# Kernel optimization log

Measured on AMD Instinct MI355X. Metric: run time of the kernel, lower is better.

The kernel has to match this reference:

```python
import jax, jax.numpy as jnp
import numpy as np

B, S, E = 4, 2048, 1024

def setup_inputs() -> dict:
    key = jax.random.key(0)
    ks = jax.random.split(key, 9)
    lim = 1.0 / np.sqrt(E)
    inp = {
        "query": jax.random.normal(ks[0], (B, S, E), dtype=jnp.float32),
        "key": jax.random.normal(ks[1], (B, S, E), dtype=jnp.float32),
        "value": jax.random.normal(ks[2], (B, S, E), dtype=jnp.float32),
        "Wq": jax.random.uniform(ks[3], (E, E), jnp.float32, -lim, lim),
        "bq": jax.random.uniform(ks[4], (E,), jnp.float32, -lim, lim),
        "Wk": jax.random.uniform(ks[5], (E, E), jnp.float32, -lim, lim),
        "bk": jax.random.uniform(ks[6], (E,), jnp.float32, -lim, lim),
        "Wv": jax.random.uniform(ks[7], (E, E), jnp.float32, -lim, lim),
        "bv": jax.random.uniform(ks[8], (E,), jnp.float32, -lim, lim),
    }
    return inp

def reference(query, key, value, Wq, bq, Wk, bk, Wv, bv):
    # Linear layers (torch stores weight as [out,in]; here W is [in,out] used as x @ W)
    q = query @ Wq + bq            # [B,S,E]
    k = key @ Wk + bk              # [B,S,E]
    v = value @ Wv + bv            # [B,S,E]
    inv_scale = jnp.asarray(E, q.dtype) ** 0.5
    scores = jnp.einsum("bse,bte->bst", q, k) / inv_scale  # [B,S,S]
    attn = jax.nn.softmax(scores, axis=-1)
    # dropout_p = 0.0 -> identity
    out = jnp.einsum("bst,bte->bse", attn, v)  # [B,S,E]
    return out
```

## Files before the change

### kernel.cpp

```cpp
#include <hip/hip_runtime.h>
#include <hip/hip_bf16.h>


typedef __bf16 bf16_t;
typedef bf16_t bf16x8 __attribute__((ext_vector_type(8)));
typedef bf16_t bf16x4 __attribute__((ext_vector_type(4)));
typedef float  f32x4  __attribute__((ext_vector_type(4)));

typedef const __attribute__((address_space(1))) unsigned gl_uint;
typedef __attribute__((address_space(3))) unsigned lds_uint;

#define BM 128
#define BN 128
#define BK 64

__device__ __forceinline__ void gload_lds16(const void* g, void* l) {
  __builtin_amdgcn_global_load_lds((gl_uint*)g, (lds_uint*)l, 16, 0, 0);
}

__device__ __forceinline__ void mfma_tile(const bf16_t* As, const bf16_t* Bs,
                                          f32x4 acc[4][4]) {
  const int lane = threadIdx.x & 63;
  const int quad = lane >> 4;
  const int l15  = lane & 15;
  const int wid  = threadIdx.x >> 6;
  const int wm   = (wid >> 1) * 64;
  const int wn   = (wid & 1) * 64;
  const int csw  = l15 & 7;
#pragma unroll
  for (int ks = 0; ks < 2; ++ks) {
    const int sg = ks * 4 + quad;
    const int c  = (sg ^ csw) * 8;
    bf16x8 fa[4], fb[4];
#pragma unroll
    for (int i = 0; i < 4; ++i)
      fa[i] = *(const bf16x8*)&As[(wm + i * 16 + l15) * BK + c];
#pragma unroll
    for (int i = 0; i < 4; ++i)
      fb[i] = *(const bf16x8*)&Bs[(wn + i * 16 + l15) * BK + c];
#pragma unroll
    for (int mi = 0; mi < 4; ++mi)
#pragma unroll
      for (int ni = 0; ni < 4; ++ni)
        acc[mi][ni] = __builtin_amdgcn_mfma_f32_16x16x32_bf16(
            fa[mi], fb[ni], acc[mi][ni], 0, 0, 0);
  }
}

__device__ __forceinline__ void gemm_core_bf16(
    const bf16_t* __restrict__ Ab, const bf16_t* __restrict__ Bb,
    const int K, bf16_t* As, bf16_t* Bs, f32x4 acc[4][4])
{
  const int tid = threadIdx.x;
  for (int kt = 0; kt < K; kt += BK) {
#pragma unroll
    for (int j = 0; j < 4; ++j) {
      const int lin = j * 256 + tid;
      const int row = lin >> 3;
      const int seg = (lin & 7) ^ (row & 7);
      gload_lds16(Ab + (size_t)row * K + kt + seg * 8, &As[lin * 8]);
    }
#pragma unroll
    for (int j = 0; j < 4; ++j) {
      const int lin = j * 256 + tid;
      const int row = lin >> 3;
      const int seg = (lin & 7) ^ (row & 7);
      gload_lds16(Bb + (size_t)row * K + kt + seg * 8, &Bs[lin * 8]);
    }
    __syncthreads();
    mfma_tile(As, Bs, acc);
    __syncthreads();
  }
}

__global__ __launch_bounds__(256, 2)
void qkv_proj(const float* __restrict__ q, const float* __restrict__ k,
              const float* __restrict__ v, const bf16_t* __restrict__ Wqt,
              const bf16_t* __restrict__ Wkt, const bf16_t* __restrict__ Wvt,
              const float* __restrict__ bq, const float* __restrict__ bk,
              const float* __restrict__ bv, bf16_t* __restrict__ qp,
              bf16_t* __restrict__ kp, bf16_t* __restrict__ vT)
{
  __shared__ __align__(16) bf16_t As[BM * BK];
  __shared__ __align__(16) bf16_t Bs[BN * BK];

  const int L = blockIdx.x;
  const int g = L >> 3;
  const int gst = (L & 7) * 3 + (g >> 6);
  const int z  = gst >> 3;
  const int sy = gst & 7;
  const int w  = g & 63;
  const int bx = w & 7;
  const int by = sy * 8 + (w >> 3);

  const float*  A    = (z == 0) ? q : (z == 1) ? k : v;
  const bf16_t* W    = (z == 0) ? Wqt : (z == 1) ? Wkt : Wvt;
  const float*  bias = (z == 0) ? bq : (z == 1) ? bk : bv;
  const int K = 1024, N = 1024;
  const float*  Ab = A + (size_t)by * BM * K;
  const bf16_t* Bb = W + (size_t)bx * BN * K;

  const int tid = threadIdx.x;

  f32x4 acc[4][4];
  const f32x4 z4 = {0.f, 0.f, 0.f, 0.f};
#pragma unroll
  for (int i = 0; i < 4; ++i)
#pragma unroll
    for (int j = 0; j < 4; ++j) acc[i][j] = z4;

  for (int kt = 0; kt < K; kt += BK) {
    float4 av[4][2];
#pragma unroll
    for (int j = 0; j < 4; ++j) {
      const int lin = j * 256 + tid;
      const int row = lin >> 3;
      const int c   = lin & 7;
      const float* gp = Ab + (size_t)row * K + kt + c * 8;
      av[j][0] = *(const float4*)gp;
      av[j][1] = *(const float4*)(gp + 4);
    }
#pragma unroll
    for (int j = 0; j < 4; ++j) {
      const int lin = j * 256 + tid;
      const int row = lin >> 3;
      const int seg = (lin & 7) ^ (row & 7);
      gload_lds16(Bb + (size_t)row * K + kt + seg * 8, &Bs[lin * 8]);
    }
#pragma unroll
    for (int j = 0; j < 4; ++j) {
      const int lin = j * 256 + tid;
      const int row = lin >> 3;
      const int c   = lin & 7;
      const int slot = c ^ (row & 7);
      bf16x8 o;
#pragma unroll
      for (int t = 0; t < 4; ++t) {
        o[t]     = (bf16_t)av[j][0][t];
        o[4 + t] = (bf16_t)av[j][1][t];
      }
      *(bf16x8*)&As[(row * 8 + slot) * 8] = o;
    }
    __syncthreads();
    mfma_tile(As, Bs, acc);
    __syncthreads();
  }

  const int lane = tid & 63;
  const int quad = lane >> 4;
  const int l15  = lane & 15;
  const int wid  = tid >> 6;
  const int wm = (wid >> 1) * 64, wn = (wid & 1) * 64;
  const int m0 = by * BM, n0 = bx * BN;
#pragma unroll
  for (int mi = 0; mi < 4; ++mi) {
#pragma unroll
    for (int ni = 0; ni < 4; ++ni) {
      const int gn = n0 + wn + ni * 16 + l15;
      const int gm = m0 + wm + mi * 16 + quad * 4;
      const float bv_ = bias[gn];
      f32x4 a = acc[mi][ni];
      if (z < 2) {
        bf16_t* C = (z == 0) ? qp : kp;
#pragma unroll
        for (int r = 0; r < 4; ++r)
          C[(size_t)(gm + r) * N + gn] = (bf16_t)(a[r] + bv_);
      } else {
        const int b = gm >> 11;
        const int s = gm & 2047;
        bf16x4 o;
#pragma unroll
        for (int r = 0; r < 4; ++r) o[r] = (bf16_t)(a[r] + bv_);
        *(bf16x4*)&vT[((size_t)b * N + gn) * 2048 + s] = o;
      }
    }
  }
}

template <int MODE>
__global__ __launch_bounds__(256, 2)
void gemm_att(const bf16_t* __restrict__ A, const bf16_t* __restrict__ Bt,
              void* __restrict__ Cv, float* __restrict__ lsum,
              const int M, const int N, const int K,
              const long long sA, const long long sB, const long long sC)
{
  __shared__ __align__(16) bf16_t As[BM * BK];
  __shared__ __align__(16) bf16_t Bs[BN * BK];

  const int L = blockIdx.x;
  int bx, by, bz;
  if (MODE == 0) {
    const int g = L >> 3;
    const int gst = (L & 7) * 2 + (g >> 6);
    bz = gst >> 2;
    const int s2 = gst & 3;
    const int w = g & 63;
    bx = (s2 & 1) * 8 + (w & 7);
    by = (s2 >> 1) * 8 + (w >> 3);
  } else {
    const int xcd = L & 7;
    const int w = (L >> 3) & 63;
    bz = xcd >> 1;
    bx = w & 7;
    by = (xcd & 1) * 8 + (w >> 3);
  }

  const bf16_t* Ab = A + (size_t)bz * sA + (size_t)by * BM * K;
  const bf16_t* Bb = Bt + (size_t)bz * sB + (size_t)bx * BN * K;

  f32x4 acc[4][4];
  const f32x4 z4 = {0.f, 0.f, 0.f, 0.f};
#pragma unroll
  for (int i = 0; i < 4; ++i)
#pragma unroll
    for (int j = 0; j < 4; ++j) acc[i][j] = z4;

  gemm_core_bf16(Ab, Bb, K, As, Bs, acc);

  const int lane = threadIdx.x & 63;
  const int quad = lane >> 4;
  const int l15  = lane & 15;
  const int wid  = threadIdx.x >> 6;
  const int wm = (wid >> 1) * 64, wn = (wid & 1) * 64;
  const int m0 = by * BM, n0 = bx * BN;

  if (MODE == 0) {
    const float cexp = 0.03125f * 1.4426950408889634f;
    bf16_t* C = (bf16_t*)Cv + (size_t)bz * sC;
    float* lrow = lsum + (size_t)bz * M;
#pragma unroll
    for (int mi = 0; mi < 4; ++mi) {
      const int gm = m0 + wm + mi * 16 + quad * 4;
      float ps[4] = {0.f, 0.f, 0.f, 0.f};
#pragma unroll
      for (int ni = 0; ni < 4; ++ni) {
        const int gn = n0 + wn + ni * 16 + l15;
        f32x4 a = acc[mi][ni];
#pragma unroll
        for (int r = 0; r < 4; ++r) {
          const float e = exp2f(a[r] * cexp);
          C[(size_t)(gm + r) * N + gn] = (bf16_t)e;
          ps[r] += e;
        }
      }
#pragma unroll
      for (int o = 1; o <= 8; o <<= 1)
#pragma unroll
        for (int r = 0; r < 4; ++r) ps[r] += __shfl_xor(ps[r], o);
      if (l15 == 0) {
#pragma unroll
        for (int r = 0; r < 4; ++r) atomicAdd(&lrow[gm + r], ps[r]);
      }
    }
  } else {
    float* C = (float*)Cv + (size_t)bz * sC;
    const float* lrow = lsum + (size_t)bz * M;
#pragma unroll
    for (int mi = 0; mi < 4; ++mi) {
      const int gm = m0 + wm + mi * 16 + quad * 4;
      float il[4];
#pragma unroll
      for (int r = 0; r < 4; ++r) il[r] = 1.0f / lrow[gm + r];
#pragma unroll
      for (int ni = 0; ni < 4; ++ni) {
        const int gn = n0 + wn + ni * 16 + l15;
        f32x4 a = acc[mi][ni];
#pragma unroll
        for (int r = 0; r < 4; ++r)
          C[(size_t)(gm + r) * N + gn] = a[r] * il[r];
      }
    }
  }
}

__global__ __launch_bounds__(256)
void transpose_cvt3(const float* __restrict__ Wq, const float* __restrict__ Wk,
                    const float* __restrict__ Wv, bf16_t* __restrict__ Wqt,
                    bf16_t* __restrict__ Wkt, bf16_t* __restrict__ Wvt) {
  const int z = blockIdx.z;
  const float* W = (z == 0) ? Wq : (z == 1) ? Wk : Wv;
  bf16_t* Wt = (z == 0) ? Wqt : (z == 1) ? Wkt : Wvt;
  __shared__ float tile[64][65];
  const int n0 = blockIdx.x * 64;
  const int k0 = blockIdx.y * 64;
  const int tid = threadIdx.x;
#pragma unroll
  for (int it = 0; it < 16; ++it) {
    const int idx = it * 256 + tid;
    const int r = idx >> 6, c = idx & 63;
    tile[r][c] = W[(size_t)(k0 + r) * 1024 + n0 + c];
  }
  __syncthreads();
#pragma unroll
  for (int it = 0; it < 16; ++it) {
    const int idx = it * 256 + tid;
    const int r = idx >> 6, c = idx & 63;
    Wt[(size_t)(n0 + r) * 1024 + k0 + c] = (bf16_t)tile[c][r];
  }
}

extern "C" void kernel_launch(void* const* d_in, const int* in_sizes, int n_in,
                              void* d_out, int out_size, void* d_ws, size_t ws_size,
                              hipStream_t stream) {
  const int B = 4, S = 2048, E = 1024;
  const size_t BSE = (size_t)B * S * E;
  const size_t EE  = (size_t)E * E;

  const float* q_in = (const float*)d_in[0];
  const float* k_in = (const float*)d_in[1];
  const float* v_in = (const float*)d_in[2];
  const float* Wq = (const float*)d_in[3];
  const float* bq = (const float*)d_in[4];
  const float* Wk = (const float*)d_in[5];
  const float* bk = (const float*)d_in[6];
  const float* Wv = (const float*)d_in[7];
  const float* bv = (const float*)d_in[8];
  float* out = (float*)d_out;

  char* ws = (char*)d_ws;
  bf16_t* Wqt = (bf16_t*)ws;
  bf16_t* Wkt = Wqt + EE;
  bf16_t* Wvt = Wkt + EE;
  bf16_t* qp  = Wvt + EE;
  bf16_t* kp  = qp + BSE;
  bf16_t* vT  = kp + BSE;
  bf16_t* P   = vT + BSE;
  float*  lsum = (float*)(P + (size_t)B * S * S);

  transpose_cvt3<<<dim3(16, 16, 3), 256, 0, stream>>>(Wq, Wk, Wv, Wqt, Wkt, Wvt);
  hipMemsetAsync(lsum, 0, (size_t)B * S * sizeof(float), stream);

  qkv_proj<<<1536, 256, 0, stream>>>(q_in, k_in, v_in, Wqt, Wkt, Wvt,
                                     bq, bk, bv, qp, kp, vT);

  gemm_att<0><<<1024, 256, 0, stream>>>(
      qp, kp, P, lsum, S, S, E,
      (long long)S * E, (long long)S * E, (long long)S * S);

  gemm_att<1><<<512, 256, 0, stream>>>(
      P, vT, out, lsum, S, E, S,
      (long long)S * S, (long long)E * S, (long long)S * E);

  (void)in_sizes; (void)n_in; (void)out_size; (void)ws_size;
}
```

Before: 313.4 us.

## Pre-convert QKV inputs to bf16 and compute softmax row sums separately

Adds a standalone kernel that converts the fp32 query/key/value activations to bf16 before the projection GEMM, so the projection can use the shared direct-to-LDS bf16 GEMM core instead of register-staged fp32 loads with in-loop conversion. It also removes the atomicAdd row-sum reduction and the memset from the score kernel, replacing them with a separate row_lsum kernel that re-reads the bf16 P matrix. This trades two extra passes over memory (writing and re-reading the bf16 activations, and re-reading P) plus extra launches for a faster projection main loop and no atomics. The row sums are now computed from bf16-rounded exponentials, which changes the rounding slightly.

```diff
diff --git a/kernel.cpp b/kernel.cpp
--- a/kernel.cpp
+++ b/kernel.cpp
@@ -74,8 +74,8 @@
 }
 
 __global__ __launch_bounds__(256, 2)
-void qkv_proj(const float* __restrict__ q, const float* __restrict__ k,
-              const float* __restrict__ v, const bf16_t* __restrict__ Wqt,
+void qkv_proj(const bf16_t* __restrict__ qb, const bf16_t* __restrict__ kb,
+              const bf16_t* __restrict__ vb, const bf16_t* __restrict__ Wqt,
               const bf16_t* __restrict__ Wkt, const bf16_t* __restrict__ Wvt,
               const float* __restrict__ bq, const float* __restrict__ bk,
               const float* __restrict__ bv, bf16_t* __restrict__ qp,
@@ -93,14 +93,12 @@
   const int bx = w & 7;
   const int by = sy * 8 + (w >> 3);
 
-  const float*  A    = (z == 0) ? q : (z == 1) ? k : v;
+  const bf16_t* A    = (z == 0) ? qb : (z == 1) ? kb : vb;
   const bf16_t* W    = (z == 0) ? Wqt : (z == 1) ? Wkt : Wvt;
   const float*  bias = (z == 0) ? bq : (z == 1) ? bk : bv;
   const int K = 1024, N = 1024;
-  const float*  Ab = A + (size_t)by * BM * K;
+  const bf16_t* Ab = A + (size_t)by * BM * K;
   const bf16_t* Bb = W + (size_t)bx * BN * K;
-
-  const int tid = threadIdx.x;
 
   f32x4 acc[4][4];
   const f32x4 z4 = {0.f, 0.f, 0.f, 0.f};
@@ -109,47 +107,12 @@
 #pragma unroll
     for (int j = 0; j < 4; ++j) acc[i][j] = z4;
 
-  for (int kt = 0; kt < K; kt += BK) {
-    float4 av[4][2];
-#pragma unroll
-    for (int j = 0; j < 4; ++j) {
-      const int lin = j * 256 + tid;
-      const int row = lin >> 3;
-      const int c   = lin & 7;
-      const float* gp = Ab + (size_t)row * K + kt + c * 8;
-      av[j][0] = *(const float4*)gp;
-      av[j][1] = *(const float4*)(gp + 4);
-    }
-#pragma unroll
-    for (int j = 0; j < 4; ++j) {
-      const int lin = j * 256 + tid;
-      const int row = lin >> 3;
-      const int seg = (lin & 7) ^ (row & 7);
-      gload_lds16(Bb + (size_t)row * K + kt + seg * 8, &Bs[lin * 8]);
-    }
-#pragma unroll
-    for (int j = 0; j < 4; ++j) {
-      const int lin = j * 256 + tid;
-      const int row = lin >> 3;
-      const int c   = lin & 7;
-      const int slot = c ^ (row & 7);
-      bf16x8 o;
-#pragma unroll
-      for (int t = 0; t < 4; ++t) {
-        o[t]     = (bf16_t)av[j][0][t];
-        o[4 + t] = (bf16_t)av[j][1][t];
-      }
-      *(bf16x8*)&As[(row * 8 + slot) * 8] = o;
-    }
-    __syncthreads();
-    mfma_tile(As, Bs, acc);
-    __syncthreads();
-  }
-
-  const int lane = tid & 63;
+  gemm_core_bf16(Ab, Bb, K, As, Bs, acc);
+
+  const int lane = threadIdx.x & 63;
   const int quad = lane >> 4;
   const int l15  = lane & 15;
-  const int wid  = tid >> 6;
+  const int wid  = threadIdx.x >> 6;
   const int wm = (wid >> 1) * 64, wn = (wid & 1) * 64;
   const int m0 = by * BM, n0 = bx * BN;
 #pragma unroll
@@ -180,7 +143,7 @@
 template <int MODE>
 __global__ __launch_bounds__(256, 2)
 void gemm_att(const bf16_t* __restrict__ A, const bf16_t* __restrict__ Bt,
-              void* __restrict__ Cv, float* __restrict__ lsum,
+              void* __restrict__ Cv, const float* __restrict__ lsum,
               const int M, const int N, const int K,
               const long long sA, const long long sB, const long long sC)
 {
@@ -227,29 +190,16 @@
   if (MODE == 0) {
     const float cexp = 0.03125f * 1.4426950408889634f;
     bf16_t* C = (bf16_t*)Cv + (size_t)bz * sC;
-    float* lrow = lsum + (size_t)bz * M;
 #pragma unroll
     for (int mi = 0; mi < 4; ++mi) {
       const int gm = m0 + wm + mi * 16 + quad * 4;
-      float ps[4] = {0.f, 0.f, 0.f, 0.f};
 #pragma unroll
       for (int ni = 0; ni < 4; ++ni) {
         const int gn = n0 + wn + ni * 16 + l15;
         f32x4 a = acc[mi][ni];
 #pragma unroll
-        for (int r = 0; r < 4; ++r) {
-          const float e = exp2f(a[r] * cexp);
-          C[(size_t)(gm + r) * N + gn] = (bf16_t)e;
-          ps[r] += e;
-        }
-      }
-#pragma unroll
-      for (int o = 1; o <= 8; o <<= 1)
-#pragma unroll
-        for (int r = 0; r < 4; ++r) ps[r] += __shfl_xor(ps[r], o);
-      if (l15 == 0) {
-#pragma unroll
-        for (int r = 0; r < 4; ++r) atomicAdd(&lrow[gm + r], ps[r]);
+        for (int r = 0; r < 4; ++r)
+          C[(size_t)(gm + r) * N + gn] = (bf16_t)exp2f(a[r] * cexp);
       }
     }
   } else {
@@ -271,6 +221,37 @@
       }
     }
   }
+}
+
+__global__ __launch_bounds__(256)
+void row_lsum(const bf16_t* __restrict__ P, float* __restrict__ lsum) {
+  const int tid = threadIdx.x, lane = tid & 63, wid = tid >> 6;
+  const size_t row = (size_t)blockIdx.x * 4 + wid;
+  const bf16_t* src = P + row * 2048;
+  float s = 0.f;
+#pragma unroll
+  for (int j = 0; j < 4; ++j) {
+    const bf16x8 v = *(const bf16x8*)&src[(j * 64 + lane) * 8];
+#pragma unroll
+    for (int t = 0; t < 8; ++t) s += (float)v[t];
+  }
+#pragma unroll
+  for (int o = 32; o; o >>= 1) s += __shfl_xor(s, o);
+  if (lane == 0) lsum[row] = s;
+}
+
+__global__ __launch_bounds__(256)
+void cvt3_k(const float* __restrict__ q, const float* __restrict__ k,
+            const float* __restrict__ v, bf16_t* __restrict__ qo,
+            bf16_t* __restrict__ ko, bf16_t* __restrict__ vo) {
+  const int z = blockIdx.y;
+  const float* in = (z == 0) ? q : (z == 1) ? k : v;
+  bf16_t* out = (z == 0) ? qo : (z == 1) ? ko : vo;
+  const size_t i = ((size_t)blockIdx.x * 256 + threadIdx.x) * 4;
+  const float4 w = *(const float4*)(in + i);
+  bf16x4 o;
+  o[0] = (bf16_t)w.x; o[1] = (bf16_t)w.y; o[2] = (bf16_t)w.z; o[3] = (bf16_t)w.w;
+  *(bf16x4*)(out + i) = o;
 }
 
 __global__ __launch_bounds__(256)
@@ -321,21 +302,26 @@
   bf16_t* Wqt = (bf16_t*)ws;
   bf16_t* Wkt = Wqt + EE;
   bf16_t* Wvt = Wkt + EE;
-  bf16_t* qp  = Wvt + EE;
+  bf16_t* qb  = Wvt + EE;
+  bf16_t* kb  = qb + BSE;
+  bf16_t* vb  = kb + BSE;
+  bf16_t* qp  = vb + BSE;
   bf16_t* kp  = qp + BSE;
   bf16_t* vT  = kp + BSE;
   bf16_t* P   = vT + BSE;
   float*  lsum = (float*)(P + (size_t)B * S * S);
 
+  cvt3_k<<<dim3(BSE / 1024, 3), 256, 0, stream>>>(q_in, k_in, v_in, qb, kb, vb);
   transpose_cvt3<<<dim3(16, 16, 3), 256, 0, stream>>>(Wq, Wk, Wv, Wqt, Wkt, Wvt);
-  hipMemsetAsync(lsum, 0, (size_t)B * S * sizeof(float), stream);
-
-  qkv_proj<<<1536, 256, 0, stream>>>(q_in, k_in, v_in, Wqt, Wkt, Wvt,
+
+  qkv_proj<<<1536, 256, 0, stream>>>(qb, kb, vb, Wqt, Wkt, Wvt,
                                      bq, bk, bv, qp, kp, vT);
 
   gemm_att<0><<<1024, 256, 0, stream>>>(
-      qp, kp, P, lsum, S, S, E,
+      qp, kp, P, nullptr, S, S, E,
       (long long)S * E, (long long)S * E, (long long)S * S);
+
+  row_lsum<<<(B * S) / 4, 256, 0, stream>>>(P, lsum);
 
   gemm_att<1><<<512, 256, 0, stream>>>(
       P, vT, out, lsum, S, E, S,
```

Measured after the change: 290.0 us. 7.5% less time.
